# Performance work log

Hardware: AMD Instinct MI355X
Metric: run time of the kernel (lower is better)

Reference implementation:

```python
import jax, jax.numpy as jnp
import numpy as np

HIDDEN = 1024
HEADS = 16
HEAD_DIM = HIDDEN // HEADS
BATCH = 2
SEQ = 2048
ROPE_BASE = 10000.0


def rotate_half(x):
    x1, x2 = x[..., : x.shape[-1] // 2], x[..., x.shape[-1] // 2 :]
    return jnp.concatenate((-x2, x1), axis=-1)


def rope_cos_sin(seq_len, dim, dtype=jnp.float32):
    inv_freq = 1.0 / (ROPE_BASE ** (jnp.arange(0, dim, 2, dtype=jnp.float32) / dim))
    t = jnp.arange(seq_len, dtype=jnp.float32)
    freqs = jnp.einsum('i,j->ij', t, inv_freq)          # [S, dim/2]
    emb = jnp.concatenate((freqs, freqs), axis=-1)       # [S, dim]
    return emb.astype(dtype).cos(), emb.astype(dtype).sin() if False else (jnp.cos(emb).astype(dtype), jnp.sin(emb).astype(dtype))[0], None


def _rope(seq_len, dim):
    inv_freq = 1.0 / (ROPE_BASE ** (jnp.arange(0, dim, 2, dtype=jnp.float32) / dim))
    t = jnp.arange(seq_len, dtype=jnp.float32)
    freqs = jnp.einsum('i,j->ij', t, inv_freq)
    emb = jnp.concatenate((freqs, freqs), axis=-1)
    return jnp.cos(emb), jnp.sin(emb)  # each [S, dim]


def setup_inputs() -> dict:
    key = jax.random.key(0)
    ks = jax.random.split(key, 9)
    scale = 1.0 / np.sqrt(HIDDEN)
    inp = {
        'hidden_states': jax.random.normal(ks[0], (BATCH, SEQ, HIDDEN), dtype=jnp.float32),
        'Wq': jax.random.uniform(ks[1], (HIDDEN, HIDDEN), minval=-scale, maxval=scale, dtype=jnp.float32),
        'bq': jax.random.uniform(ks[2], (HIDDEN,), minval=-scale, maxval=scale, dtype=jnp.float32),
        'Wk': jax.random.uniform(ks[3], (HIDDEN, HIDDEN), minval=-scale, maxval=scale, dtype=jnp.float32),
        'bk': jax.random.uniform(ks[4], (HIDDEN,), minval=-scale, maxval=scale, dtype=jnp.float32),
        'Wv': jax.random.uniform(ks[5], (HIDDEN, HIDDEN), minval=-scale, maxval=scale, dtype=jnp.float32),
        'bv': jax.random.uniform(ks[6], (HIDDEN,), minval=-scale, maxval=scale, dtype=jnp.float32),
        'Wo': jax.random.uniform(ks[7], (HIDDEN, HIDDEN), minval=-scale, maxval=scale, dtype=jnp.float32),
        'bo': jax.random.uniform(ks[8], (HIDDEN,), minval=-scale, maxval=scale, dtype=jnp.float32),
    }
    return inp


def reference(hidden_states, Wq, bq, Wk, bk, Wv, bv, Wo, bo):
    B, S, H = hidden_states.shape
    # projections (torch Linear: x @ W.T + b), split into heads: [B, nH, S, hd]
    def proj(W, b):
        y = hidden_states @ W.T + b
        return y.reshape(B, S, HEADS, HEAD_DIM).transpose(0, 2, 1, 3)

    q = proj(Wq, bq)
    k = proj(Wk, bk)
    v = proj(Wv, bv)

    cos, sin = _rope(S, HEAD_DIM)  # [S, hd], broadcast over B, nH
    q = q * cos + rotate_half(q) * sin
    k = k * cos + rotate_half(k) * sin

    scale = 1.0 / jnp.sqrt(jnp.array(HEAD_DIM, dtype=q.dtype))
    logits = jnp.einsum('bhqd,bhkd->bhqk', q, k) * scale  # [B, nH, S, S]
    attn = jax.nn.softmax(logits, axis=-1)
    out = jnp.einsum('bhqk,bhkd->bhqd', attn, v)           # [B, nH, S, hd]
    out = out.transpose(0, 2, 1, 3).reshape(B, S, H)
    return out @ Wo.T + bo
```

## Files before the change

kernel.cpp:

```cpp
#include <hip/hip_runtime.h>
#include <hip/hip_bf16.h>
#include <math.h>

#define HIDDEN 1024
#define NH 16
#define HD 64
#define BATCH 2
#define SEQ 2048

typedef __attribute__((ext_vector_type(8))) short bf16x8;
typedef __attribute__((ext_vector_type(4))) float f32x4;

static __device__ __forceinline__ unsigned short f2b(float f) {
    __hip_bfloat16 h = __float2bfloat16(f);
    return __builtin_bit_cast(unsigned short, h);
}

static __device__ __forceinline__ float fexp2(float x) {
    return __builtin_amdgcn_exp2f(x);
}

static __device__ __forceinline__ void async16(const unsigned short* g, unsigned short* l) {
    __builtin_amdgcn_global_load_lds(
        (const __attribute__((address_space(1))) unsigned int*)g,
        (__attribute__((address_space(3))) unsigned int*)l, 16, 0, 0);
}

__global__ __launch_bounds__(256)
void cvt_bf16(const float* __restrict__ X,
              const float* __restrict__ Wq, const float* __restrict__ Wk,
              const float* __restrict__ Wv, const float* __restrict__ Wo,
              unsigned short* __restrict__ dst)
{
    const size_t g = (size_t)blockIdx.x * 256 + threadIdx.x;
    const float* src;
    size_t local;
    if (g < 1048576) {
        src = X; local = g;
    } else {
        const size_t gg = g - 1048576;
        const int r = (int)(gg >> 18);
        local = gg & 262143;
        src = (r == 0) ? Wq : ((r == 1) ? Wk : ((r == 2) ? Wv : Wo));
    }
    const float4 v = *(const float4*)(src + local * 4);
    ushort4 o;
    o.x = f2b(v.x); o.y = f2b(v.y); o.z = f2b(v.z); o.w = f2b(v.w);
    *(ushort4*)(dst + g * 4) = o;
}

__global__ __launch_bounds__(256, 3)
void qkv_rope(const unsigned short* __restrict__ X,
              const unsigned short* __restrict__ Wqb, const float* __restrict__ bq,
              const unsigned short* __restrict__ Wkb, const float* __restrict__ bk,
              const unsigned short* __restrict__ Wvb, const float* __restrict__ bv,
              unsigned short* __restrict__ qw, unsigned short* __restrict__ kw,
              unsigned short* __restrict__ vw)
{
    const int proj = blockIdx.y >> 3;
    const unsigned short* W = (proj == 0) ? Wqb : ((proj == 1) ? Wkb : Wvb);
    const float* bias       = (proj == 0) ? bq : ((proj == 1) ? bk : bv);
    unsigned short* outp    = (proj == 0) ? qw : ((proj == 1) ? kw : vw);
    const int tn = (blockIdx.y & 7) * 128;
    const int tm = blockIdx.x * 128;

    __shared__ __align__(16) unsigned short As[128 * 64];
    __shared__ __align__(16) unsigned short Bs[128 * 64];

    const int tid  = threadIdx.x;
    const int lane = tid & 63;
    const int wave = tid >> 6;
    const int quad = lane >> 4;
    const int l16  = lane & 15;
    const int wm   = (wave & 1) * 64;
    const int wn   = (wave >> 1) * 64;

    const int srow = tid >> 3;
    const int sccx = (tid & 7) ^ (srow & 7);
    const unsigned short* Ag = X + (size_t)(tm + srow) * HIDDEN + sccx * 8;
    const unsigned short* Bg = W + (size_t)(tn + srow) * HIDDEN + sccx * 8;
    unsigned short* lA = As + tid * 8;
    unsigned short* lB = Bs + tid * 8;

    f32x4 acc[4][4] = {};

    for (int k0 = 0; k0 < HIDDEN; k0 += 64) {
        __syncthreads();
#pragma unroll
        for (int p = 0; p < 4; ++p) {
            async16(Ag + k0 + p * 32 * HIDDEN, lA + p * 2048);
            async16(Bg + k0 + p * 32 * HIDDEN, lB + p * 2048);
        }
        __syncthreads();
#pragma unroll
        for (int c = 0; c < 2; ++c) {
            bf16x8 af[4], bfr[4];
#pragma unroll
            for (int i = 0; i < 4; ++i) {
                const int row = wm + i * 16 + l16;
                af[i] = *(const bf16x8*)(As + row * 64 + (((c * 4 + quad) ^ (l16 & 7)) * 8));
            }
#pragma unroll
            for (int j = 0; j < 4; ++j) {
                const int row = wn + j * 16 + l16;
                bfr[j] = *(const bf16x8*)(Bs + row * 64 + (((c * 4 + quad) ^ (l16 & 7)) * 8));
            }
#pragma unroll
            for (int i = 0; i < 4; ++i)
#pragma unroll
                for (int j = 0; j < 4; ++j)
                    acc[i][j] = __builtin_amdgcn_mfma_f32_16x16x32_bf16(af[i], bfr[j], acc[i][j], 0, 0, 0);
        }
    }

    const bool dorope = (proj < 2);
    float bsv[4];
#pragma unroll
    for (int j = 0; j < 4; ++j) bsv[j] = bias[tn + wn + j * 16 + l16];
    float inv_e = 0.f, inv_o = 0.f;
    if (dorope) {
        const float LB = 0.4152410118609203f;
        inv_e = exp2f(-LB * (float)l16);
        inv_o = exp2f(-LB * (float)(16 + l16));
    }
#pragma unroll
    for (int i = 0; i < 4; ++i) {
#pragma unroll
        for (int r = 0; r < 4; ++r) {
            const int m = tm + wm + i * 16 + quad * 4 + r;
            const int b = m >> 11;
            const int s = m & (SEQ - 1);
            float cs0 = 1.f, sn0 = 0.f, cs1 = 1.f, sn1 = 0.f;
            if (dorope) {
                const float sf = (float)s;
                __sincosf(sf * inv_e, &sn0, &cs0);
                __sincosf(sf * inv_o, &sn1, &cs1);
            }
#pragma unroll
            for (int j = 0; j < 4; ++j) {
                const int n = tn + wn + j * 16 + l16;
                const float v = acc[i][j][r] + bsv[j];
                float o = v;
                if (dorope) {
                    const float vp = acc[i][j ^ 2][r] + bsv[j ^ 2];
                    o = v * ((j & 1) ? cs1 : cs0) + ((j < 2) ? -vp : vp) * ((j & 1) ? sn1 : sn0);
                }
                const int h = n >> 6;
                const int d = n & 63;
                outp[(((size_t)(b * NH + h)) * SEQ + s) * HD + d] = f2b(o);
            }
        }
    }
}

__global__ __launch_bounds__(256, 2)
void attn_fwd(const unsigned short* __restrict__ qb, const unsigned short* __restrict__ kb,
              const unsigned short* __restrict__ vb, unsigned short* __restrict__ ob)
{
    const int flat  = blockIdx.y * gridDim.x + blockIdx.x;
    const int flat2 = (flat & 7) * 64 + (flat >> 3);
    const int bh = flat2 >> 4;
    const int qt = flat2 & 15;
    const int b  = bh >> 4;
    const int h  = bh & 15;
    const unsigned short* Q = qb + (size_t)bh * SEQ * HD;
    const unsigned short* K = kb + (size_t)bh * SEQ * HD;
    const unsigned short* V = vb + (size_t)bh * SEQ * HD;

    const int tid  = threadIdx.x;
    const int wave = tid >> 6;
    const int lane = tid & 63;
    const int quad = lane >> 4;
    const int l16  = lane & 15;
    const int q0   = qt * 128 + wave * 32;

    __shared__ __align__(16) unsigned short Pb[4][32 * 136];
    __shared__ __align__(16) unsigned short Vt[2][64 * 136];

    bf16x8 qf[2][2];
#pragma unroll
    for (int mt = 0; mt < 2; ++mt)
#pragma unroll
        for (int kk = 0; kk < 2; ++kk)
            qf[mt][kk] = *(const bf16x8*)(Q + (size_t)(q0 + mt * 16 + l16) * HD + kk * 32 + quad * 8);

    f32x4 oacc[2][4] = {};
    float mr[2][4], lr[2][4];
#pragma unroll
    for (int mt = 0; mt < 2; ++mt)
#pragma unroll
        for (int r = 0; r < 4; ++r) { mr[mt][r] = -3.0e38f; lr[mt][r] = 0.f; }

    const int vkey = tid >> 3;
    const int vd0  = (tid & 7) * 8;
    const int vm   = tid & 7;

    const float KSCL = 0.18033688011112042f;

    for (int kt = 0; kt < SEQ / 128; ++kt) {
        const int t0  = kt * 128;
        const int buf = kt & 1;

        f32x4 sc[2][8] = {};
#pragma unroll
        for (int kk = 0; kk < 2; ++kk) {
            bf16x8 kf[8];
#pragma unroll
            for (int jj = 0; jj < 8; ++jj)
                kf[jj] = *(const bf16x8*)(K + (size_t)(t0 + jj * 16 + l16) * HD + kk * 32 + quad * 8);
#pragma unroll
            for (int mt = 0; mt < 2; ++mt)
#pragma unroll
                for (int jj = 0; jj < 8; ++jj)
                    sc[mt][jj] = __builtin_amdgcn_mfma_f32_16x16x32_bf16(qf[mt][kk], kf[jj], sc[mt][jj], 0, 0, 0);
        }

#pragma unroll
        for (int p = 0; p < 4; ++p) {
            const int ky = vkey + 32 * p;
            const int cs = ky ^ (vm << 3);
            bf16x8 vv = *(const bf16x8*)(V + (size_t)(t0 + ky) * HD + vd0);
#pragma unroll
            for (int u = 0; u < 8; ++u)
                Vt[buf][(vd0 + u) * 136 + cs] = ((const unsigned short*)&vv)[u];
        }

        float dmax = -3.0e38f;
#pragma unroll
        for (int mt = 0; mt < 2; ++mt) {
#pragma unroll
            for (int r = 0; r < 4; ++r) {
                float mx = sc[mt][0][r];
#pragma unroll
                for (int jj = 1; jj < 8; ++jj) mx = fmaxf(mx, sc[mt][jj][r]);
                dmax = fmaxf(dmax, fmaf(mx, KSCL, -mr[mt][r]));
            }
        }
        if (!__all(dmax <= 8.0f)) {
#pragma unroll
            for (int mt = 0; mt < 2; ++mt) {
#pragma unroll
                for (int r = 0; r < 4; ++r) {
                    float mx = sc[mt][0][r];
#pragma unroll
                    for (int jj = 1; jj < 8; ++jj) mx = fmaxf(mx, sc[mt][jj][r]);
                    float ms = mx * KSCL;
#pragma unroll
                    for (int off = 8; off; off >>= 1) ms = fmaxf(ms, __shfl_xor(ms, off));
                    const float mnew  = fmaxf(mr[mt][r], ms);
                    const float alpha = fexp2(mr[mt][r] - mnew);
                    mr[mt][r] = mnew;
                    lr[mt][r] *= alpha;
#pragma unroll
                    for (int nn = 0; nn < 4; ++nn) oacc[mt][nn][r] *= alpha;
                }
            }
        }
#pragma unroll
        for (int mt = 0; mt < 2; ++mt) {
#pragma unroll
            for (int r = 0; r < 4; ++r) {
                const float mnew = mr[mt][r];
                float ps = 0.f;
                const int prow = (mt * 16 + quad * 4 + r) * 136;
#pragma unroll
                for (int jj = 0; jj < 8; ++jj) {
                    const float p = fexp2(fmaf(sc[mt][jj][r], KSCL, -mnew));
                    ps += p;
                    Pb[wave][prow + jj * 16 + l16] = f2b(p);
                }
                lr[mt][r] += ps;
            }
        }

        __syncthreads();

#pragma unroll
        for (int kk2 = 0; kk2 < 4; ++kk2) {
            bf16x8 pf[2], vf[4];
#pragma unroll
            for (int mt = 0; mt < 2; ++mt)
                pf[mt] = *(const bf16x8*)(&Pb[wave][(mt * 16 + l16) * 136 + kk2 * 32 + quad * 8]);
#pragma unroll
            for (int nn = 0; nn < 4; ++nn) {
                const int d   = nn * 16 + l16;
                const int mrd = (nn * 2 + (l16 >> 3)) & 7;
                const int cb  = (kk2 * 32 + quad * 8) ^ (mrd << 3);
                vf[nn] = *(const bf16x8*)(&Vt[buf][d * 136 + cb]);
            }
#pragma unroll
            for (int mt = 0; mt < 2; ++mt)
#pragma unroll
                for (int nn = 0; nn < 4; ++nn)
                    oacc[mt][nn] = __builtin_amdgcn_mfma_f32_16x16x32_bf16(pf[mt], vf[nn], oacc[mt][nn], 0, 0, 0);
        }
    }

#pragma unroll
    for (int mt = 0; mt < 2; ++mt) {
#pragma unroll
        for (int r = 0; r < 4; ++r) {
            float ls = lr[mt][r];
#pragma unroll
            for (int off = 8; off; off >>= 1) ls += __shfl_xor(ls, off);
            const float inv = 1.0f / ls;
            const int s = q0 + mt * 16 + quad * 4 + r;
#pragma unroll
            for (int nn = 0; nn < 4; ++nn) {
                const int d = nn * 16 + l16;
                ob[((size_t)(b * SEQ + s)) * HIDDEN + h * HD + d] = f2b(oacc[mt][nn][r] * inv);
            }
        }
    }
}

__global__ __launch_bounds__(256, 4)
void out_proj(const unsigned short* __restrict__ A,
              const unsigned short* __restrict__ W,
              const float* __restrict__ bias,
              float* __restrict__ out)
{
    const int tn = blockIdx.y * 64;
    const int tm = blockIdx.x * 64;

    __shared__ __align__(16) unsigned short As[64 * 64];
    __shared__ __align__(16) unsigned short Bs[64 * 64];

    const int tid  = threadIdx.x;
    const int lane = tid & 63;
    const int wave = tid >> 6;
    const int quad = lane >> 4;
    const int l16  = lane & 15;
    const int wm   = (wave & 1) * 32;
    const int wn   = (wave >> 1) * 32;

    const int srow = tid >> 3;
    const int sccx = (tid & 7) ^ (srow & 7);
    const unsigned short* Ag = A + (size_t)(tm + srow) * HIDDEN + sccx * 8;
    const unsigned short* Bg = W + (size_t)(tn + srow) * HIDDEN + sccx * 8;
    unsigned short* lA = As + tid * 8;
    unsigned short* lB = Bs + tid * 8;

    f32x4 acc[2][2] = {};

    for (int k0 = 0; k0 < HIDDEN; k0 += 64) {
        __syncthreads();
#pragma unroll
        for (int p = 0; p < 2; ++p) {
            async16(Ag + k0 + p * 32 * HIDDEN, lA + p * 2048);
            async16(Bg + k0 + p * 32 * HIDDEN, lB + p * 2048);
        }
        __syncthreads();
#pragma unroll
        for (int c = 0; c < 2; ++c) {
            bf16x8 af[2], bfr[2];
#pragma unroll
            for (int i = 0; i < 2; ++i) {
                const int row = wm + i * 16 + l16;
                af[i] = *(const bf16x8*)(As + row * 64 + (((c * 4 + quad) ^ (l16 & 7)) * 8));
            }
#pragma unroll
            for (int j = 0; j < 2; ++j) {
                const int row = wn + j * 16 + l16;
                bfr[j] = *(const bf16x8*)(Bs + row * 64 + (((c * 4 + quad) ^ (l16 & 7)) * 8));
            }
#pragma unroll
            for (int i = 0; i < 2; ++i)
#pragma unroll
                for (int j = 0; j < 2; ++j)
                    acc[i][j] = __builtin_amdgcn_mfma_f32_16x16x32_bf16(af[i], bfr[j], acc[i][j], 0, 0, 0);
        }
    }

    float bsv[2];
#pragma unroll
    for (int j = 0; j < 2; ++j) bsv[j] = bias[tn + wn + j * 16 + l16];
#pragma unroll
    for (int i = 0; i < 2; ++i) {
#pragma unroll
        for (int r = 0; r < 4; ++r) {
            const int m = tm + wm + i * 16 + quad * 4 + r;
#pragma unroll
            for (int j = 0; j < 2; ++j) {
                const int n = tn + wn + j * 16 + l16;
                out[(size_t)m * HIDDEN + n] = acc[i][j][r] + bsv[j];
            }
        }
    }
}

extern "C" void kernel_launch(void* const* d_in, const int* in_sizes, int n_in,
                              void* d_out, int out_size, void* d_ws, size_t ws_size,
                              hipStream_t stream) {
    const float* hs = (const float*)d_in[0];
    const float* Wq = (const float*)d_in[1];
    const float* bq = (const float*)d_in[2];
    const float* Wk = (const float*)d_in[3];
    const float* bk = (const float*)d_in[4];
    const float* Wv = (const float*)d_in[5];
    const float* bv = (const float*)d_in[6];
    const float* Wo = (const float*)d_in[7];
    const float* bo = (const float*)d_in[8];
    float* out = (float*)d_out;

    unsigned short* Xb  = (unsigned short*)d_ws;
    unsigned short* Wqb = Xb + 4194304;
    unsigned short* Wkb = Wqb + 1048576;
    unsigned short* Wvb = Wkb + 1048576;
    unsigned short* Wob = Wvb + 1048576;
    unsigned short* qw  = Wob + 1048576;
    unsigned short* kw  = qw + 4194304;
    unsigned short* vw  = kw + 4194304;
    unsigned short* aw  = vw + 4194304;

    cvt_bf16<<<dim3(8192), 256, 0, stream>>>(hs, Wq, Wk, Wv, Wo, Xb);
    qkv_rope<<<dim3(32, 24), 256, 0, stream>>>(Xb, Wqb, bq, Wkb, bk, Wvb, bv, qw, kw, vw);
    attn_fwd<<<dim3(16, 32), 256, 0, stream>>>(qw, kw, vw, aw);
    out_proj<<<dim3(64, 16), 256, 0, stream>>>(aw, Wob, bo, out);
}
```

Baseline: 208.7 us.

## Double-buffer weight tiles in LDS and read activations directly from global

The QKV projection GEMM now keeps only the weight (B) tile in LDS, double-buffered so the next k-slice's async load overlaps the current MFMA work, with one barrier per iteration instead of two. The activation (A) fragments are loaded straight from global memory into registers instead of being staged through LDS. This is meant to cut LDS traffic and barrier stalls and to hide load latency. The risk is that direct global A loads are less coalesced and their latency is exposed, because each A row is reused by two waves and across the eight column-block groups.

```diff
diff --git a/kernel.cpp b/kernel.cpp
--- a/kernel.cpp
+++ b/kernel.cpp
@@ -64,8 +64,7 @@
     const int tn = (blockIdx.y & 7) * 128;
     const int tm = blockIdx.x * 128;
 
-    __shared__ __align__(16) unsigned short As[128 * 64];
-    __shared__ __align__(16) unsigned short Bs[128 * 64];
+    __shared__ __align__(16) unsigned short Bs[2][128 * 64];
 
     const int tid  = threadIdx.x;
     const int lane = tid & 63;
@@ -77,33 +76,44 @@
 
     const int srow = tid >> 3;
     const int sccx = (tid & 7) ^ (srow & 7);
-    const unsigned short* Ag = X + (size_t)(tm + srow) * HIDDEN + sccx * 8;
     const unsigned short* Bg = W + (size_t)(tn + srow) * HIDDEN + sccx * 8;
-    unsigned short* lA = As + tid * 8;
-    unsigned short* lB = Bs + tid * 8;
+
+    const unsigned short* Arow[4];
+#pragma unroll
+    for (int i = 0; i < 4; ++i)
+        Arow[i] = X + (size_t)(tm + wm + i * 16 + l16) * HIDDEN + quad * 8;
 
     f32x4 acc[4][4] = {};
 
-    for (int k0 = 0; k0 < HIDDEN; k0 += 64) {
-        __syncthreads();
-#pragma unroll
-        for (int p = 0; p < 4; ++p) {
-            async16(Ag + k0 + p * 32 * HIDDEN, lA + p * 2048);
-            async16(Bg + k0 + p * 32 * HIDDEN, lB + p * 2048);
-        }
-        __syncthreads();
+    {
+        unsigned short* lB = &Bs[0][tid * 8];
+#pragma unroll
+        for (int p = 0; p < 4; ++p)
+            async16(Bg + p * 32 * HIDDEN, lB + p * 2048);
+    }
+    __syncthreads();
+
+    for (int t = 0; t < 16; ++t) {
+        const int k0  = t * 64;
+        const int cur = t & 1;
+
+        if (t < 15) {
+            unsigned short* lB = &Bs[cur ^ 1][tid * 8];
+#pragma unroll
+            for (int p = 0; p < 4; ++p)
+                async16(Bg + (k0 + 64) + p * 32 * HIDDEN, lB + p * 2048);
+        }
+
 #pragma unroll
         for (int c = 0; c < 2; ++c) {
             bf16x8 af[4], bfr[4];
 #pragma unroll
-            for (int i = 0; i < 4; ++i) {
-                const int row = wm + i * 16 + l16;
-                af[i] = *(const bf16x8*)(As + row * 64 + (((c * 4 + quad) ^ (l16 & 7)) * 8));
-            }
+            for (int i = 0; i < 4; ++i)
+                af[i] = *(const bf16x8*)(Arow[i] + k0 + c * 32);
 #pragma unroll
             for (int j = 0; j < 4; ++j) {
                 const int row = wn + j * 16 + l16;
-                bfr[j] = *(const bf16x8*)(Bs + row * 64 + (((c * 4 + quad) ^ (l16 & 7)) * 8));
+                bfr[j] = *(const bf16x8*)(&Bs[cur][row * 64 + (((c * 4 + quad) ^ (l16 & 7)) * 8)]);
             }
 #pragma unroll
             for (int i = 0; i < 4; ++i)
@@ -111,6 +121,8 @@
                 for (int j = 0; j < 4; ++j)
                     acc[i][j] = __builtin_amdgcn_mfma_f32_16x16x32_bf16(af[i], bfr[j], acc[i][j], 0, 0, 0);
         }
+
+        __syncthreads();
     }
 
     const bool dorope = (proj < 2);
```

New measurement: 237.7 us. +13.9%, slower.

## Fuse Q/K/V projections per head so each block shares its X tile across all three

Applied to the files above, without the earlier changes.

The QKV kernel now assigns each block one head (64 output columns) for all three projections at once, loading the X tile once and three 64-row weight tiles per k-step instead of one 128-row weight tile per projection. This lowers X tile re-reads from global memory (512 blocks instead of 768) and lets each block compute the RoPE sin/cos once for both Q and K. In exchange it uses more LDS and accumulator registers (launch bounds drop from 3 to 2 blocks per CU), and the grid is smaller.

```diff
diff --git a/kernel.cpp b/kernel.cpp
--- a/kernel.cpp
+++ b/kernel.cpp
@@ -49,7 +49,7 @@
     *(ushort4*)(dst + g * 4) = o;
 }
 
-__global__ __launch_bounds__(256, 3)
+__global__ __launch_bounds__(256, 2)
 void qkv_rope(const unsigned short* __restrict__ X,
               const unsigned short* __restrict__ Wqb, const float* __restrict__ bq,
               const unsigned short* __restrict__ Wkb, const float* __restrict__ bk,
@@ -57,15 +57,12 @@
               unsigned short* __restrict__ qw, unsigned short* __restrict__ kw,
               unsigned short* __restrict__ vw)
 {
-    const int proj = blockIdx.y >> 3;
-    const unsigned short* W = (proj == 0) ? Wqb : ((proj == 1) ? Wkb : Wvb);
-    const float* bias       = (proj == 0) ? bq : ((proj == 1) ? bk : bv);
-    unsigned short* outp    = (proj == 0) ? qw : ((proj == 1) ? kw : vw);
-    const int tn = (blockIdx.y & 7) * 128;
+    const int tn = blockIdx.y * 64;
+    const int h  = blockIdx.y;
     const int tm = blockIdx.x * 128;
 
     __shared__ __align__(16) unsigned short As[128 * 64];
-    __shared__ __align__(16) unsigned short Bs[128 * 64];
+    __shared__ __align__(16) unsigned short Bs[3][64 * 64];
 
     const int tid  = threadIdx.x;
     const int lane = tid & 63;
@@ -73,55 +70,63 @@
     const int quad = lane >> 4;
     const int l16  = lane & 15;
     const int wm   = (wave & 1) * 64;
-    const int wn   = (wave >> 1) * 64;
+    const int w2   = wave >> 1;
 
     const int srow = tid >> 3;
     const int sccx = (tid & 7) ^ (srow & 7);
-    const unsigned short* Ag = X + (size_t)(tm + srow) * HIDDEN + sccx * 8;
-    const unsigned short* Bg = W + (size_t)(tn + srow) * HIDDEN + sccx * 8;
+    const unsigned short* Ag  = X   + (size_t)(tm + srow) * HIDDEN + sccx * 8;
+    const unsigned short* Bg0 = Wqb + (size_t)(tn + srow) * HIDDEN + sccx * 8;
+    const unsigned short* Bg1 = Wkb + (size_t)(tn + srow) * HIDDEN + sccx * 8;
+    const unsigned short* Bg2 = Wvb + (size_t)(tn + srow) * HIDDEN + sccx * 8;
     unsigned short* lA = As + tid * 8;
-    unsigned short* lB = Bs + tid * 8;
-
-    f32x4 acc[4][4] = {};
+
+    f32x4 acc[3][4][2] = {};
 
     for (int k0 = 0; k0 < HIDDEN; k0 += 64) {
         __syncthreads();
 #pragma unroll
-        for (int p = 0; p < 4; ++p) {
+        for (int p = 0; p < 4; ++p)
             async16(Ag + k0 + p * 32 * HIDDEN, lA + p * 2048);
-            async16(Bg + k0 + p * 32 * HIDDEN, lB + p * 2048);
+#pragma unroll
+        for (int p = 0; p < 2; ++p) {
+            async16(Bg0 + k0 + p * 32 * HIDDEN, &Bs[0][tid * 8 + p * 2048]);
+            async16(Bg1 + k0 + p * 32 * HIDDEN, &Bs[1][tid * 8 + p * 2048]);
+            async16(Bg2 + k0 + p * 32 * HIDDEN, &Bs[2][tid * 8 + p * 2048]);
         }
         __syncthreads();
 #pragma unroll
         for (int c = 0; c < 2; ++c) {
-            bf16x8 af[4], bfr[4];
+            const int csw = ((c * 4 + quad) ^ (l16 & 7)) * 8;
+            bf16x8 af[4];
 #pragma unroll
             for (int i = 0; i < 4; ++i) {
                 const int row = wm + i * 16 + l16;
-                af[i] = *(const bf16x8*)(As + row * 64 + (((c * 4 + quad) ^ (l16 & 7)) * 8));
-            }
-#pragma unroll
-            for (int j = 0; j < 4; ++j) {
-                const int row = wn + j * 16 + l16;
-                bfr[j] = *(const bf16x8*)(Bs + row * 64 + (((c * 4 + quad) ^ (l16 & 7)) * 8));
-            }
-#pragma unroll
-            for (int i = 0; i < 4; ++i)
-#pragma unroll
-                for (int j = 0; j < 4; ++j)
-                    acc[i][j] = __builtin_amdgcn_mfma_f32_16x16x32_bf16(af[i], bfr[j], acc[i][j], 0, 0, 0);
-        }
-    }
-
-    const bool dorope = (proj < 2);
-    float bsv[4];
-#pragma unroll
-    for (int j = 0; j < 4; ++j) bsv[j] = bias[tn + wn + j * 16 + l16];
-    float inv_e = 0.f, inv_o = 0.f;
-    if (dorope) {
-        const float LB = 0.4152410118609203f;
-        inv_e = exp2f(-LB * (float)l16);
-        inv_o = exp2f(-LB * (float)(16 + l16));
+                af[i] = *(const bf16x8*)(As + row * 64 + csw);
+            }
+#pragma unroll
+            for (int pr = 0; pr < 3; ++pr) {
+                bf16x8 bfr[2];
+#pragma unroll
+                for (int j = 0; j < 2; ++j) {
+                    const int row = j * 32 + w2 * 16 + l16;
+                    bfr[j] = *(const bf16x8*)(&Bs[pr][row * 64 + csw]);
+                }
+#pragma unroll
+                for (int i = 0; i < 4; ++i)
+#pragma unroll
+                    for (int j = 0; j < 2; ++j)
+                        acc[pr][i][j] = __builtin_amdgcn_mfma_f32_16x16x32_bf16(af[i], bfr[j], acc[pr][i][j], 0, 0, 0);
+            }
+        }
+    }
+
+    const float LB = 0.4152410118609203f;
+    const float invf = exp2f(-LB * (float)(w2 * 16 + l16));
+    float bsv[3][2];
+#pragma unroll
+    for (int j = 0; j < 2; ++j) {
+        const int n = tn + j * 32 + w2 * 16 + l16;
+        bsv[0][j] = bq[n]; bsv[1][j] = bk[n]; bsv[2][j] = bv[n];
     }
 #pragma unroll
     for (int i = 0; i < 4; ++i) {
@@ -130,24 +135,23 @@
             const int m = tm + wm + i * 16 + quad * 4 + r;
             const int b = m >> 11;
             const int s = m & (SEQ - 1);
-            float cs0 = 1.f, sn0 = 0.f, cs1 = 1.f, sn1 = 0.f;
-            if (dorope) {
-                const float sf = (float)s;
-                __sincosf(sf * inv_e, &sn0, &cs0);
-                __sincosf(sf * inv_o, &sn1, &cs1);
-            }
-#pragma unroll
-            for (int j = 0; j < 4; ++j) {
-                const int n = tn + wn + j * 16 + l16;
-                const float v = acc[i][j][r] + bsv[j];
-                float o = v;
-                if (dorope) {
-                    const float vp = acc[i][j ^ 2][r] + bsv[j ^ 2];
-                    o = v * ((j & 1) ? cs1 : cs0) + ((j < 2) ? -vp : vp) * ((j & 1) ? sn1 : sn0);
+            float sn, cs;
+            __sincosf((float)s * invf, &sn, &cs);
+            const size_t obase = (((size_t)(b * NH + h)) * SEQ + s) * HD;
+#pragma unroll
+            for (int j = 0; j < 2; ++j) {
+                const int d = j * 32 + w2 * 16 + l16;
+                {
+                    const float v0 = acc[0][i][j][r] + bsv[0][j];
+                    const float vp = acc[0][i][j ^ 1][r] + bsv[0][j ^ 1];
+                    qw[obase + d] = f2b(v0 * cs + (j ? vp : -vp) * sn);
                 }
-                const int h = n >> 6;
-                const int d = n & 63;
-                outp[(((size_t)(b * NH + h)) * SEQ + s) * HD + d] = f2b(o);
+                {
+                    const float v0 = acc[1][i][j][r] + bsv[1][j];
+                    const float vp = acc[1][i][j ^ 1][r] + bsv[1][j ^ 1];
+                    kw[obase + d] = f2b(v0 * cs + (j ? vp : -vp) * sn);
+                }
+                vw[obase + d] = f2b(acc[2][i][j][r] + bsv[2][j]);
             }
         }
     }
@@ -414,7 +418,7 @@
     unsigned short* aw  = vw + 4194304;
 
     cvt_bf16<<<dim3(8192), 256, 0, stream>>>(hs, Wq, Wk, Wv, Wo, Xb);
-    qkv_rope<<<dim3(32, 24), 256, 0, stream>>>(Xb, Wqb, bq, Wkb, bk, Wvb, bv, qw, kw, vw);
+    qkv_rope<<<dim3(32, 16), 256, 0, stream>>>(Xb, Wqb, bq, Wkb, bk, Wvb, bv, qw, kw, vw);
     attn_fwd<<<dim3(16, 32), 256, 0, stream>>>(qw, kw, vw, aw);
     out_proj<<<dim3(64, 16), 256, 0, stream>>>(aw, Wob, bo, out);
 }
```

Result: no change. 211.1 us (+1.2%).
